# Optimization experiments

Measured on AMD Instinct MI355X. Metric: run time of the kernel, lower is better.

Reference implementation:

```python
import jax, jax.numpy as jnp
import numpy as np


def _unfold(x, ks, pad):
    # torch nn.Unfold ordering: flattened channel dim is (c, kh, kw), output (b, c*ks*ks, h*w)
    b, c, h, w = x.shape
    if ks == 1:
        return x.reshape(b, c, h * w)
    xp = jnp.pad(x, ((0, 0), (0, 0), (pad, pad), (pad, pad)))
    patches = jnp.stack([xp[:, :, i:i + h, j:j + w] for i in range(ks) for j in range(ks)], axis=2)  # (b,c,ks*ks,h,w)
    return patches.reshape(b, c * ks * ks, h * w)


def _cg_conv(x, weight, ce_w, gd_w, gd2_w, ci_w, ks, pad, g=8):
    # Content-gated conv: SE-style dynamic kernel generation + unfold + batched matmul
    b, c, h, w = x.shape
    oc = weight.shape[0]
    # AdaptiveMaxPool2d((ks,ks)); h,w divisible by ks so bins are uniform
    gl = x.reshape(b, c, ks, h // ks, ks, w // ks).max(axis=(3, 5)).reshape(b, c, ks * ks)
    ce2 = jnp.einsum('bck,nk->bcn', gl, ce_w)                      # (b,c,num_lat)
    out = jnp.einsum('bcn,kn->bck', jax.nn.relu(ce2), gd_w)        # (b,c,ks*ks)
    # channel path: (b,c//g,g,num_lat) -> transpose -> Linear(g -> oc/(c//g))
    t = jax.nn.relu(jnp.transpose(ce2.reshape(b, c // g, g, -1), (0, 1, 3, 2)))
    ocp = jnp.transpose(jnp.einsum('bpng,og->bpno', t, ci_w), (0, 1, 3, 2)).reshape(b, oc, -1)
    ocp = jnp.einsum('bon,kn->bok', jax.nn.relu(ocp), gd2_w)       # (b,oc,ks*ks)
    dyn = jax.nn.sigmoid(out[:, None, :, :] + ocp[:, :, None, :])  # (b,oc,c,ks*ks)
    dyn = dyn * weight.reshape(1, oc, c, ks * ks)
    x_un = _unfold(x, ks, pad)                                     # (b, c*ks*ks, h*w)
    y = jnp.einsum('bok,bkl->bol', dyn.reshape(b, oc, c * ks * ks), x_un)
    return y.reshape(b, oc, h, w)


def setup_inputs() -> dict:
    key = jax.random.key(0)
    ks_ = jax.random.split(key, 12)
    b, c_in, c_hid, c_out, H, W = 4, 64, 256, 64, 96, 96
    s = 0.02
    inp = {
        'x': jax.random.normal(ks_[0], (b, c_in, H, W), jnp.float32),
        # fc1: 1x1, num_lat = 1, ci: 8 -> 256//(64//8)=32
        'fc1_weight': jax.random.normal(ks_[1], (c_hid, c_in, 1, 1), jnp.float32) * s,
        'fc1_ce': jax.random.normal(ks_[2], (1, 1), jnp.float32) * s,
        'fc1_gd': jax.random.normal(ks_[3], (1, 1), jnp.float32) * s,
        'fc1_gd2': jax.random.normal(ks_[4], (1, 1), jnp.float32) * s,
        'fc1_ci': jax.random.normal(ks_[5], (32, 8), jnp.float32) * s,
        # fc2: 3x3, num_lat = 5, ci: 8 -> 64//(256//8)=2
        'fc2_weight': jax.random.normal(ks_[6], (c_out, c_hid, 3, 3), jnp.float32) * s,
        'fc2_ce': jax.random.normal(ks_[7], (5, 9), jnp.float32) * s,
        'fc2_gd': jax.random.normal(ks_[8], (9, 5), jnp.float32) * s,
        'fc2_gd2': jax.random.normal(ks_[9], (9, 5), jnp.float32) * s,
        'fc2_ci': jax.random.normal(ks_[10], (2, 8), jnp.float32) * s,
    }
    return inp


def reference(x, fc1_weight, fc1_ce, fc1_gd, fc1_gd2, fc1_ci,
              fc2_weight, fc2_ce, fc2_gd, fc2_gd2, fc2_ci):
    h = _cg_conv(x, fc1_weight, fc1_ce, fc1_gd, fc1_gd2, fc1_ci, ks=1, pad=0)
    h = jax.nn.gelu(h, approximate=False)  # torch nn.GELU default is exact erf
    return _cg_conv(h, fc2_weight, fc2_ce, fc2_gd, fc2_gd2, fc2_ci, ks=3, pad=1)
```

## Files before the change

### kernel.cpp

```cpp
#include <hip/hip_runtime.h>
#include <math.h>

typedef __attribute__((ext_vector_type(8))) short short8x;
typedef __attribute__((ext_vector_type(4))) float float4x;
typedef unsigned short u16;
typedef unsigned int u32;

__device__ __forceinline__ float bf2f(u16 u) {
    return __uint_as_float(((u32)u) << 16);
}
__device__ __forceinline__ u16 f2bf(float f) {
    u32 u = __float_as_uint(f);
    u32 r = (u + 0x7fffu + ((u >> 16) & 1u)) >> 16;
    return (u16)r;
}


__global__ __launch_bounds__(256) void k_gl1(const float* __restrict__ x, float* __restrict__ gl1,
                                             u32* __restrict__ h2p32) {
    if (blockIdx.x >= 256) {
        int t = threadIdx.x;
        u32* plane = h2p32 + (blockIdx.x - 256) * (98 * 98 * 16);
        for (int i = t; i < 1568; i += 256) plane[i] = 0u;
        for (int i = t; i < 1568; i += 256) plane[97 * 98 * 16 + i] = 0u;
        for (int i = t; i < 3072; i += 256) {
            int r = (i >> 5) + 1;
            int p = ((i >> 4) & 1) * 97;
            int w = i & 15;
            plane[(r * 98 + p) * 16 + w] = 0u;
        }
        return;
    }
    int b = blockIdx.x >> 6, c = blockIdx.x & 63;
    const float4* p = (const float4*)(x + (b * 64 + c) * 9216);
    float m = -1e30f;
    #pragma unroll
    for (int i = 0; i < 9; i++) {
        float4 v = p[i * 256 + threadIdx.x];
        m = fmaxf(m, fmaxf(fmaxf(v.x, v.y), fmaxf(v.z, v.w)));
    }
    __shared__ float red[256];
    red[threadIdx.x] = m;
    __syncthreads();
    for (int s = 128; s > 0; s >>= 1) {
        if (threadIdx.x < s) red[threadIdx.x] = fmaxf(red[threadIdx.x], red[threadIdx.x + s]);
        __syncthreads();
    }
    if (threadIdx.x == 0) gl1[b * 64 + c] = red[0];
}

__global__ __launch_bounds__(256) void k_gate1(const float* __restrict__ gl1,
                                               const float* __restrict__ ce, const float* __restrict__ gd,
                                               const float* __restrict__ gd2, const float* __restrict__ ci,
                                               const float* __restrict__ w1, u16* __restrict__ W1A) {
    int b = blockIdx.x, t = threadIdx.x;
    __shared__ float rce[64], out1[64], ocp[256];
    float cew = ce[0], gdw = gd[0], gd2w = gd2[0];
    if (t < 64) {
        float r = fmaxf(gl1[b * 64 + t] * cew, 0.f);
        rce[t] = r;
        out1[t] = r * gdw;
    }
    __syncthreads();
    {
        int p = t >> 5, oi = t & 31;
        float s = 0.f;
        #pragma unroll
        for (int g = 0; g < 8; g++) s += rce[p * 8 + g] * ci[oi * 8 + g];
        ocp[t] = fmaxf(s, 0.f) * gd2w;
    }
    __syncthreads();
    u16* Wb = W1A + b * 256 * 64;
    for (int idx = t; idx < 256 * 64; idx += 256) {
        int o = idx >> 6, c = idx & 63;
        float v = out1[c] + ocp[o];
        float sg = 1.f / (1.f + expf(-v));
        Wb[idx] = f2bf(sg * w1[idx]);
    }
}

__global__ __launch_bounds__(256) void k_gemm1(const u16* __restrict__ W1A, const float* __restrict__ x,
                                               u16* __restrict__ h2p, float* __restrict__ pm) {
    int bi = blockIdx.x;
    int b = bi / 192, rem = bi % 192;
    int y = rem >> 1, half = rem & 1;
    int t = threadIdx.x, wave = t >> 6, lane = t & 63, l15 = lane & 15, quad = lane >> 4;

    __shared__ __align__(16) u16 xs[48 * 72];
    const float* xb = x + (b * 64) * 9216 + y * 96 + half * 48;
    #pragma unroll
    for (int i = 0; i < 12; i++) {
        int idx = i * 256 + t;
        int c = idx / 48, px = idx - c * 48;
        xs[px * 72 + c] = f2bf(xb[c * 9216 + px]);
    }
    __syncthreads();

    float4x acc[4][3];
    #pragma unroll
    for (int mt = 0; mt < 4; mt++)
        #pragma unroll
        for (int nt = 0; nt < 3; nt++) acc[mt][nt] = (float4x){0.f, 0.f, 0.f, 0.f};
    const u16* Wb = W1A + b * 256 * 64;
    #pragma unroll
    for (int c0 = 0; c0 < 64; c0 += 32) {
        short8x bfr[3];
        #pragma unroll
        for (int nt = 0; nt < 3; nt++)
            bfr[nt] = *(const short8x*)(xs + (nt * 16 + l15) * 72 + c0 + quad * 8);
        #pragma unroll
        for (int mt = 0; mt < 4; mt++) {
            int oc = wave * 64 + mt * 16 + l15;
            short8x afr = *(const short8x*)(Wb + oc * 64 + c0 + quad * 8);
            #pragma unroll
            for (int nt = 0; nt < 3; nt++)
                acc[mt][nt] = __builtin_amdgcn_mfma_f32_16x16x32_bf16(afr, bfr[nt], acc[mt][nt], 0, 0, 0);
        }
    }
    const float is2 = 0.70710678118654752f;
    float gf[4][3][4];
    #pragma unroll
    for (int mt = 0; mt < 4; mt++) {
        #pragma unroll
        for (int nt = 0; nt < 3; nt++) {
            int xx = half * 48 + nt * 16 + l15;
            int oc0 = wave * 64 + mt * 16 + quad * 4;
            int g = oc0 >> 5, cl = oc0 & 31;
            u16 pk[4];
            #pragma unroll
            for (int r = 0; r < 4; r++) {
                float v = acc[mt][nt][r];
                float gl = 0.5f * v * (1.f + erff(v * is2));
                gf[mt][nt][r] = gl;
                pk[r] = f2bf(gl);
            }
            u16* dst = h2p + ((((b * 8 + g) * 98 + y + 1) * 98) + xx + 1) * 32 + cl;
            *(ushort4*)dst = make_ushort4(pk[0], pk[1], pk[2], pk[3]);
        }
    }
    #pragma unroll
    for (int mt = 0; mt < 4; mt++) {
        float vA[4], vB[4];
        #pragma unroll
        for (int r = 0; r < 4; r++) {
            if (half == 0) { vA[r] = fmaxf(gf[mt][0][r], gf[mt][1][r]); vB[r] = gf[mt][2][r]; }
            else           { vA[r] = gf[mt][0][r]; vB[r] = fmaxf(gf[mt][1][r], gf[mt][2][r]); }
        }
        #pragma unroll
        for (int m = 1; m < 16; m <<= 1) {
            #pragma unroll
            for (int r = 0; r < 4; r++) {
                vA[r] = fmaxf(vA[r], __shfl_xor(vA[r], m));
                vB[r] = fmaxf(vB[r], __shfl_xor(vB[r], m));
            }
        }
        if (l15 == 0) {
            float* base = pm + ((b * 96 + y) * 4 + half * 2) * 256;
            #pragma unroll
            for (int r = 0; r < 4; r++) {
                int oc = wave * 64 + mt * 16 + quad * 4 + r;
                base[oc] = vA[r];
                base[256 + oc] = vB[r];
            }
        }
    }
}

__global__ __launch_bounds__(256) void k_gate2(const float* __restrict__ pm,
                                               const float* __restrict__ ce, const float* __restrict__ gd,
                                               const float* __restrict__ gd2, const float* __restrict__ ci,
                                               const float* __restrict__ w2, u16* __restrict__ W2A) {
    int b = blockIdx.x >> 4, s = blockIdx.x & 15;
    int t = threadIdx.x;
    __shared__ float rce[256][5];
    __shared__ float out2[256][9];
    __shared__ float ocp2[64][9];
    {
        float gl[9];
        #pragma unroll
        for (int ki = 0; ki < 3; ki++) {
            float b0 = -1e30f, b1 = -1e30f, b2 = -1e30f;
            for (int yy = 0; yy < 32; yy++) {
                const float* p = pm + ((b * 96 + ki * 32 + yy) * 4) * 256 + t;
                b0 = fmaxf(b0, p[0]);
                b1 = fmaxf(b1, fmaxf(p[256], p[512]));
                b2 = fmaxf(b2, p[768]);
            }
            gl[ki * 3 + 0] = b0; gl[ki * 3 + 1] = b1; gl[ki * 3 + 2] = b2;
        }
        float r[5];
        #pragma unroll
        for (int n = 0; n < 5; n++) {
            float sv = 0.f;
            #pragma unroll
            for (int k = 0; k < 9; k++) sv += gl[k] * ce[n * 9 + k];
            r[n] = fmaxf(sv, 0.f);
            rce[t][n] = r[n];
        }
        #pragma unroll
        for (int k = 0; k < 9; k++) {
            float sv = 0.f;
            #pragma unroll
            for (int n = 0; n < 5; n++) sv += r[n] * gd[k * 5 + n];
            out2[t][k] = sv;
        }
    }
    __syncthreads();
    if (t < 64) {
        int p = t >> 1, oi = t & 1;
        float rt[5];
        #pragma unroll
        for (int n = 0; n < 5; n++) {
            float sv = 0.f;
            #pragma unroll
            for (int g = 0; g < 8; g++) sv += rce[p * 8 + g][n] * ci[oi * 8 + g];
            rt[n] = fmaxf(sv, 0.f);
        }
        #pragma unroll
        for (int k = 0; k < 9; k++) {
            float sv = 0.f;
            #pragma unroll
            for (int n = 0; n < 5; n++) sv += rt[n] * gd2[k * 5 + n];
            ocp2[t][k] = sv;
        }
    }
    __syncthreads();
    u16* Wb = W2A + b * (8 * 9 * 64 * 32);
    for (int it = 0; it < 36; it++) {
        int flat = s * 9216 + it * 256 + t;
        int cl = flat & 31;
        int o = (flat >> 5) & 63;
        int rest = flat >> 11;
        int k = rest % 9, g = rest / 9;
        int c = g * 32 + cl;
        float v = out2[c][k] + ocp2[o][k];
        float sg = 1.f / (1.f + expf(-v));
        Wb[flat] = f2bf(sg * w2[(o * 256 + c) * 9 + k]);
    }
}

__global__ __launch_bounds__(256) void k_conv2(const u16* __restrict__ W2A, const u16* __restrict__ h2p,
                                               float* __restrict__ out) {
    int b = blockIdx.x / 96, y = blockIdx.x % 96;
    int t = threadIdx.x, wave = t >> 6, lane = t & 63, l15 = lane & 15, quad = lane >> 4;
    int mi = wave & 1, ni = wave >> 1;
    __shared__ __align__(16) u16 Als[9 * 64 * 32];
    __shared__ __align__(16) u16 Bls[3 * 98 * 32];
    float4x acc[2][3];
    #pragma unroll
    for (int mt = 0; mt < 2; mt++)
        #pragma unroll
        for (int nt = 0; nt < 3; nt++) acc[mt][nt] = (float4x){0.f, 0.f, 0.f, 0.f};

    for (int g = 0; g < 8; g++) {
        __syncthreads();
        const uint4* As = (const uint4*)(W2A + (b * 8 + g) * (9 * 64 * 32));
        uint4* Ad = (uint4*)Als;
        #pragma unroll
        for (int i = 0; i < 9; i++) Ad[t + i * 256] = As[t + i * 256];
        #pragma unroll
        for (int r = 0; r < 3; r++) {
            const uint4* Bs = (const uint4*)(h2p + (((b * 8 + g) * 98 + y + r) * 98) * 32);
            uint4* Bd = (uint4*)(Bls + r * 98 * 32);
            for (int i = t; i < 392; i += 256) Bd[i] = Bs[i];
        }
        __syncthreads();
        #pragma unroll
        for (int k = 0; k < 9; k++) {
            int ki = k / 3, kj = k - ki * 3;
            short8x af0 = *(const short8x*)(Als + (k * 64 + mi * 32 + l15) * 32 + quad * 8);
            short8x af1 = *(const short8x*)(Als + (k * 64 + mi * 32 + 16 + l15) * 32 + quad * 8);
            #pragma unroll
            for (int nt = 0; nt < 3; nt++) {
                int px = ni * 48 + nt * 16 + l15 + kj;
                short8x bf = *(const short8x*)(Bls + (ki * 98 + px) * 32 + quad * 8);
                acc[0][nt] = __builtin_amdgcn_mfma_f32_16x16x32_bf16(af0, bf, acc[0][nt], 0, 0, 0);
                acc[1][nt] = __builtin_amdgcn_mfma_f32_16x16x32_bf16(af1, bf, acc[1][nt], 0, 0, 0);
            }
        }
    }
    #pragma unroll
    for (int mt = 0; mt < 2; mt++) {
        #pragma unroll
        for (int nt = 0; nt < 3; nt++) {
            int xx = ni * 48 + nt * 16 + l15;
            #pragma unroll
            for (int r = 0; r < 4; r++) {
                int oc = mi * 32 + mt * 16 + quad * 4 + r;
                out[((b * 64 + oc) * 96 + y) * 96 + xx] = acc[mt][nt][r];
            }
        }
    }
}

extern "C" void kernel_launch(void* const* d_in, const int* in_sizes, int n_in,
                              void* d_out, int out_size, void* d_ws, size_t ws_size,
                              hipStream_t stream) {
    const float* x    = (const float*)d_in[0];
    const float* w1   = (const float*)d_in[1];
    const float* ce1  = (const float*)d_in[2];
    const float* gd1  = (const float*)d_in[3];
    const float* gd21 = (const float*)d_in[4];
    const float* ci1  = (const float*)d_in[5];
    const float* w2   = (const float*)d_in[6];
    const float* ce2  = (const float*)d_in[7];
    const float* gd2  = (const float*)d_in[8];
    const float* gd22 = (const float*)d_in[9];
    const float* ci2  = (const float*)d_in[10];
    float* out = (float*)d_out;

    char* ws = (char*)d_ws;
    u16*   h2p  = (u16*)(ws + 4718592);
    u16*   W1A  = (u16*)(ws + 24387584);
    u16*   W2A  = (u16*)(ws + 24518656);
    float* gl1  = (float*)(ws + 25698304);
    float* pm   = (float*)(ws + 25796608);

    k_gl1  <<<288, 256, 0, stream>>>(x, gl1, (u32*)h2p);
    k_gate1<<<4,   256, 0, stream>>>(gl1, ce1, gd1, gd21, ci1, w1, W1A);
    k_gemm1<<<768, 256, 0, stream>>>(W1A, x, h2p, pm);
    k_gate2<<<64,  256, 0, stream>>>(pm, ce2, gd2, gd22, ci2, w2, W2A);
    k_conv2<<<384, 256, 0, stream>>>(W2A, h2p, out);
}
```

Baseline: 149.8 us.

## Fuse gate2 max-pool via atomicMax, widen gate1 grid, halve conv2 block

gemm1 now folds its per-row GELU maxima straight into a 9-bin global max buffer with order-preserving uint atomicMax. gate2 therefore reads only 9 values per channel instead of scanning the per-row partial maxima. The buffer is zeroed in k_gl1. gate1 is split over 64 blocks instead of 4 to parallelise the sigmoid weight build. conv2 drops to 128 threads per block with each wave covering all 64 output channels, which doubles the MFMA work per B-fragment load but halves the threads per block and raises register pressure.

```diff
diff --git a/kernel.cpp b/kernel.cpp
--- a/kernel.cpp
+++ b/kernel.cpp
@@ -14,13 +14,22 @@
     u32 r = (u + 0x7fffu + ((u >> 16) & 1u)) >> 16;
     return (u16)r;
 }
+__device__ __forceinline__ u32 fenc(float f) {
+    u32 b = __float_as_uint(f);
+    return b ^ (0x80000000u | (u32)((int)b >> 31));
+}
+__device__ __forceinline__ float fdec(u32 u) {
+    u32 b = (u & 0x80000000u) ? (u ^ 0x80000000u) : ~u;
+    return __uint_as_float(b);
+}
 
 
 __global__ __launch_bounds__(256) void k_gl1(const float* __restrict__ x, float* __restrict__ gl1,
-                                             u32* __restrict__ h2p32) {
+                                             u32* __restrict__ h2p32, u32* __restrict__ gl2u) {
     if (blockIdx.x >= 256) {
         int t = threadIdx.x;
-        u32* plane = h2p32 + (blockIdx.x - 256) * (98 * 98 * 16);
+        int plane_id = blockIdx.x - 256;
+        u32* plane = h2p32 + plane_id * (98 * 98 * 16);
         for (int i = t; i < 1568; i += 256) plane[i] = 0u;
         for (int i = t; i < 1568; i += 256) plane[97 * 98 * 16 + i] = 0u;
         for (int i = t; i < 3072; i += 256) {
@@ -29,6 +38,8 @@
             int w = i & 15;
             plane[(r * 98 + p) * 16 + w] = 0u;
         }
+        for (int i = plane_id * 288 + t; i < (plane_id + 1) * 288; i += 256)
+            gl2u[i] = 0u;
         return;
     }
     int b = blockIdx.x >> 6, c = blockIdx.x & 63;
@@ -53,7 +64,8 @@
                                                const float* __restrict__ ce, const float* __restrict__ gd,
                                                const float* __restrict__ gd2, const float* __restrict__ ci,
                                                const float* __restrict__ w1, u16* __restrict__ W1A) {
-    int b = blockIdx.x, t = threadIdx.x;
+    int b = blockIdx.x >> 4, s = blockIdx.x & 15;
+    int t = threadIdx.x;
     __shared__ float rce[64], out1[64], ocp[256];
     float cew = ce[0], gdw = gd[0], gd2w = gd2[0];
     if (t < 64) {
@@ -64,14 +76,16 @@
     __syncthreads();
     {
         int p = t >> 5, oi = t & 31;
-        float s = 0.f;
-        #pragma unroll
-        for (int g = 0; g < 8; g++) s += rce[p * 8 + g] * ci[oi * 8 + g];
-        ocp[t] = fmaxf(s, 0.f) * gd2w;
+        float sv = 0.f;
+        #pragma unroll
+        for (int g = 0; g < 8; g++) sv += rce[p * 8 + g] * ci[oi * 8 + g];
+        ocp[t] = fmaxf(sv, 0.f) * gd2w;
     }
     __syncthreads();
     u16* Wb = W1A + b * 256 * 64;
-    for (int idx = t; idx < 256 * 64; idx += 256) {
+    #pragma unroll
+    for (int i = 0; i < 4; i++) {
+        int idx = s * 1024 + i * 256 + t;
         int o = idx >> 6, c = idx & 63;
         float v = out1[c] + ocp[o];
         float sg = 1.f / (1.f + expf(-v));
@@ -80,7 +94,7 @@
 }
 
 __global__ __launch_bounds__(256) void k_gemm1(const u16* __restrict__ W1A, const float* __restrict__ x,
-                                               u16* __restrict__ h2p, float* __restrict__ pm) {
+                                               u16* __restrict__ h2p, u32* __restrict__ gl2u) {
     int bi = blockIdx.x;
     int b = bi / 192, rem = bi % 192;
     int y = rem >> 1, half = rem & 1;
@@ -138,6 +152,9 @@
             *(ushort4*)dst = make_ushort4(pk[0], pk[1], pk[2], pk[3]);
         }
     }
+    int ki = y >> 5;
+    int kA = ki * 3 + (half == 0 ? 0 : 1);
+    int kB = ki * 3 + (half == 0 ? 1 : 2);
     #pragma unroll
     for (int mt = 0; mt < 4; mt++) {
         float vA[4], vB[4];
@@ -155,18 +172,17 @@
             }
         }
         if (l15 == 0) {
-            float* base = pm + ((b * 96 + y) * 4 + half * 2) * 256;
             #pragma unroll
             for (int r = 0; r < 4; r++) {
                 int oc = wave * 64 + mt * 16 + quad * 4 + r;
-                base[oc] = vA[r];
-                base[256 + oc] = vB[r];
-            }
-        }
-    }
-}
-
-__global__ __launch_bounds__(256) void k_gate2(const float* __restrict__ pm,
+                atomicMax(&gl2u[(b * 9 + kA) * 256 + oc], fenc(vA[r]));
+                atomicMax(&gl2u[(b * 9 + kB) * 256 + oc], fenc(vB[r]));
+            }
+        }
+    }
+}
+
+__global__ __launch_bounds__(256) void k_gate2(const u32* __restrict__ gl2u,
                                                const float* __restrict__ ce, const float* __restrict__ gd,
                                                const float* __restrict__ gd2, const float* __restrict__ ci,
                                                const float* __restrict__ w2, u16* __restrict__ W2A) {
@@ -178,16 +194,7 @@
     {
         float gl[9];
         #pragma unroll
-        for (int ki = 0; ki < 3; ki++) {
-            float b0 = -1e30f, b1 = -1e30f, b2 = -1e30f;
-            for (int yy = 0; yy < 32; yy++) {
-                const float* p = pm + ((b * 96 + ki * 32 + yy) * 4) * 256 + t;
-                b0 = fmaxf(b0, p[0]);
-                b1 = fmaxf(b1, fmaxf(p[256], p[512]));
-                b2 = fmaxf(b2, p[768]);
-            }
-            gl[ki * 3 + 0] = b0; gl[ki * 3 + 1] = b1; gl[ki * 3 + 2] = b2;
-        }
+        for (int k = 0; k < 9; k++) gl[k] = fdec(gl2u[(b * 9 + k) * 256 + t]);
         float r[5];
         #pragma unroll
         for (int n = 0; n < 5; n++) {
@@ -239,16 +246,15 @@
     }
 }
 
-__global__ __launch_bounds__(256) void k_conv2(const u16* __restrict__ W2A, const u16* __restrict__ h2p,
+__global__ __launch_bounds__(128) void k_conv2(const u16* __restrict__ W2A, const u16* __restrict__ h2p,
                                                float* __restrict__ out) {
     int b = blockIdx.x / 96, y = blockIdx.x % 96;
-    int t = threadIdx.x, wave = t >> 6, lane = t & 63, l15 = lane & 15, quad = lane >> 4;
-    int mi = wave & 1, ni = wave >> 1;
+    int t = threadIdx.x, ni = t >> 6, lane = t & 63, l15 = lane & 15, quad = lane >> 4;
     __shared__ __align__(16) u16 Als[9 * 64 * 32];
     __shared__ __align__(16) u16 Bls[3 * 98 * 32];
-    float4x acc[2][3];
-    #pragma unroll
-    for (int mt = 0; mt < 2; mt++)
+    float4x acc[4][3];
+    #pragma unroll
+    for (int mt = 0; mt < 4; mt++)
         #pragma unroll
         for (int nt = 0; nt < 3; nt++) acc[mt][nt] = (float4x){0.f, 0.f, 0.f, 0.f};
 
@@ -257,36 +263,39 @@
         const uint4* As = (const uint4*)(W2A + (b * 8 + g) * (9 * 64 * 32));
         uint4* Ad = (uint4*)Als;
         #pragma unroll
-        for (int i = 0; i < 9; i++) Ad[t + i * 256] = As[t + i * 256];
+        for (int i = 0; i < 18; i++) Ad[t + i * 128] = As[t + i * 128];
         #pragma unroll
         for (int r = 0; r < 3; r++) {
             const uint4* Bs = (const uint4*)(h2p + (((b * 8 + g) * 98 + y + r) * 98) * 32);
             uint4* Bd = (uint4*)(Bls + r * 98 * 32);
-            for (int i = t; i < 392; i += 256) Bd[i] = Bs[i];
+            for (int i = t; i < 392; i += 128) Bd[i] = Bs[i];
         }
         __syncthreads();
         #pragma unroll
         for (int k = 0; k < 9; k++) {
             int ki = k / 3, kj = k - ki * 3;
-            short8x af0 = *(const short8x*)(Als + (k * 64 + mi * 32 + l15) * 32 + quad * 8);
-            short8x af1 = *(const short8x*)(Als + (k * 64 + mi * 32 + 16 + l15) * 32 + quad * 8);
+            short8x af[4];
+            #pragma unroll
+            for (int mt = 0; mt < 4; mt++)
+                af[mt] = *(const short8x*)(Als + (k * 64 + mt * 16 + l15) * 32 + quad * 8);
             #pragma unroll
             for (int nt = 0; nt < 3; nt++) {
                 int px = ni * 48 + nt * 16 + l15 + kj;
                 short8x bf = *(const short8x*)(Bls + (ki * 98 + px) * 32 + quad * 8);
-                acc[0][nt] = __builtin_amdgcn_mfma_f32_16x16x32_bf16(af0, bf, acc[0][nt], 0, 0, 0);
-                acc[1][nt] = __builtin_amdgcn_mfma_f32_16x16x32_bf16(af1, bf, acc[1][nt], 0, 0, 0);
-            }
-        }
-    }
-    #pragma unroll
-    for (int mt = 0; mt < 2; mt++) {
+                #pragma unroll
+                for (int mt = 0; mt < 4; mt++)
+                    acc[mt][nt] = __builtin_amdgcn_mfma_f32_16x16x32_bf16(af[mt], bf, acc[mt][nt], 0, 0, 0);
+            }
+        }
+    }
+    #pragma unroll
+    for (int mt = 0; mt < 4; mt++) {
         #pragma unroll
         for (int nt = 0; nt < 3; nt++) {
             int xx = ni * 48 + nt * 16 + l15;
             #pragma unroll
             for (int r = 0; r < 4; r++) {
-                int oc = mi * 32 + mt * 16 + quad * 4 + r;
+                int oc = mt * 16 + quad * 4 + r;
                 out[((b * 64 + oc) * 96 + y) * 96 + xx] = acc[mt][nt][r];
             }
         }
@@ -314,11 +323,11 @@
     u16*   W1A  = (u16*)(ws + 24387584);
     u16*   W2A  = (u16*)(ws + 24518656);
     float* gl1  = (float*)(ws + 25698304);
-    float* pm   = (float*)(ws + 25796608);
-
-    k_gl1  <<<288, 256, 0, stream>>>(x, gl1, (u32*)h2p);
-    k_gate1<<<4,   256, 0, stream>>>(gl1, ce1, gd1, gd21, ci1, w1, W1A);
-    k_gemm1<<<768, 256, 0, stream>>>(W1A, x, h2p, pm);
-    k_gate2<<<64,  256, 0, stream>>>(pm, ce2, gd2, gd22, ci2, w2, W2A);
-    k_conv2<<<384, 256, 0, stream>>>(W2A, h2p, out);
-}
+    u32*   gl2u = (u32*)(ws + 25796608);
+
+    k_gl1  <<<288, 256, 0, stream>>>(x, gl1, (u32*)h2p, gl2u);
+    k_gate1<<<64,  256, 0, stream>>>(gl1, ce1, gd1, gd21, ci1, w1, W1A);
+    k_gemm1<<<768, 256, 0, stream>>>(W1A, x, h2p, gl2u);
+    k_gate2<<<64,  256, 0, stream>>>(gl2u, ce2, gd2, gd22, ci2, w2, W2A);
+    k_conv2<<<384, 128, 0, stream>>>(W2A, h2p, out);
+}
```

Result: slower. 154.8 us (+3.3%).
